# Performance work log

Hardware: AMD Instinct MI355X
Metric: run time of the kernel (lower is better)

The kernel has to match this reference:

```python
import jax, jax.numpy as jnp
import numpy as np

DIST_THD = 1.0   # config.dist_thd
EPS = 1e-8       # matches torch.nn.functional.cosine_similarity eps


def setup_inputs() -> dict:
    key = jax.random.key(0)
    k1, k2 = jax.random.split(key)
    async_fea = jax.random.normal(k1, (64, 512, 128), dtype=jnp.float32)  # [B, N, D]
    coord = jax.random.normal(k2, (64, 512, 2), dtype=jnp.float32)        # [B, N, 2]
    return {"async_fea": async_fea, "coord": coord}


def reference(async_fea, coord):
    B, N, _ = async_fea.shape
    # pairwise cosine similarity: normalize rows, then batched matmul
    norms = jnp.maximum(jnp.linalg.norm(async_fea, axis=-1, keepdims=True), EPS)
    fn = async_fea / norms
    cos = jnp.einsum('bid,bjd->bij', fn, fn)  # [B, N, N]

    # pairwise euclidean distance on coords
    diff = coord[:, :, None, :] - coord[:, None, :, :]  # [B, N, N, 2]
    d2 = jnp.sum(diff * diff, axis=-1)                   # [B, N, N]
    eye = jnp.eye(N, dtype=d2.dtype)
    # add eye before sqrt so the (zeroed-out) diagonal stays sqrt-safe
    dist = jnp.sqrt(d2 + eye)
    off_diag = 1.0 - eye

    async_adj = cos * jnp.exp(-dist / DIST_THD) * off_diag
    sync_adj = jnp.where(dist < DIST_THD, 1.0, 0.0) * off_diag
    return jnp.stack([async_adj, sync_adj])  # [2, B, N, N]
```

## Files before the change

### kernel.cpp

```cpp
#include <hip/hip_runtime.h>
#include <hip/hip_bf16.h>

typedef short bf16x8 __attribute__((ext_vector_type(8)));
typedef float f32x4  __attribute__((ext_vector_type(4)));

#define NB 64
#define NN 512
#define DD 128

__device__ __forceinline__ unsigned short f2bf(float f) {
    unsigned int u = __float_as_uint(f);
    unsigned int r = (u + 0x7FFFu + ((u >> 16) & 1u)) >> 16;
    return (unsigned short)r;
}

__global__ __launch_bounds__(256) void ASG_norm_kernel(
    const float* __restrict__ fea, unsigned int* __restrict__ fn)
{
    const int id   = blockIdx.x;
    const int xcd  = id & 7;
    const int q    = id >> 3;
    const int b    = xcd + 8 * (q >> 5);
    const int t    = q & 31;
    const int wid  = threadIdx.x >> 6;
    const int lane = threadIdx.x & 63;
    const int row0 = b * NN + t * 16 + wid * 4;
    const float2* src = reinterpret_cast<const float2*>(fea);

    float2 v[4];
    float  s[4];
#pragma unroll
    for (int rr = 0; rr < 4; ++rr) {
        v[rr] = src[(size_t)(row0 + rr) * (DD / 2) + lane];
        s[rr] = v[rr].x * v[rr].x + v[rr].y * v[rr].y;
    }
#pragma unroll
    for (int o = 32; o; o >>= 1) {
#pragma unroll
        for (int rr = 0; rr < 4; ++rr) s[rr] += __shfl_xor(s[rr], o);
    }
#pragma unroll
    for (int rr = 0; rr < 4; ++rr) {
        const float scale = 1.0f / fmaxf(sqrtf(s[rr]), 1e-8f);
        const unsigned short a = f2bf(v[rr].x * scale);
        const unsigned short bb = f2bf(v[rr].y * scale);
        fn[(size_t)(row0 + rr) * (DD / 2) + lane] =
            (unsigned int)a | ((unsigned int)bb << 16);
    }
}

__global__ __launch_bounds__(256, 4) void ASG_adj_kernel(
    const unsigned short* __restrict__ fn, const float* __restrict__ coord,
    float* __restrict__ out)
{
    const int id  = blockIdx.x;
    const int xcd = id & 7;
    const int q   = id >> 3;
    const int b   = xcd + 8 * (q >> 5);
    const int t   = q & 31;
    const int bi  = t >> 3;
    const int bj  = t & 7;

    const int tid = threadIdx.x;
    const int wid = tid >> 6, lane = tid & 63;
    const int wr  = wid >> 1, wc = wid & 1;
    const int row0 = bi * 128 + wr * 64;
    const int col0 = bj * 64  + wc * 32;
    const int lo = lane & 15, hi = lane >> 4;

    __shared__ float2 crow[128];
    __shared__ float2 ccol[64];
    __shared__ float  xpose[4][16 * 36];

    const float2* cb = reinterpret_cast<const float2*>(coord) + (size_t)b * NN;
    if (tid < 128)      crow[tid] = cb[bi * 128 + tid];
    else if (tid < 192) ccol[tid - 128] = cb[bj * 64 + (tid - 128)];
    __syncthreads();

    const unsigned short* fb = fn + (size_t)b * NN * DD;
    const int lk = hi * 8;

    bf16x8 bfrag[2][4];
#pragma unroll
    for (int n = 0; n < 2; ++n) {
        const unsigned short* p = fb + (size_t)(col0 + n * 16 + lo) * DD + lk;
#pragma unroll
        for (int kk = 0; kk < 4; ++kk)
            bfrag[n][kk] = *reinterpret_cast<const bf16x8*>(p + kk * 32);
    }

    float* outA = out + (size_t)b * NN * NN;
    float* outS = out + (size_t)NB * NN * NN + (size_t)b * NN * NN;
    float* xp = xpose[wid];

    const int c4 = (lane & 7) * 4;
    const int jbase = col0 + c4;
    float2 cj[4];
#pragma unroll
    for (int q2 = 0; q2 < 4; ++q2) cj[q2] = ccol[wc * 32 + c4 + q2];

#define LOADA(DST, MM)                                                        \
    {                                                                         \
        const unsigned short* p =                                             \
            fb + (size_t)(row0 + (MM) * 16 + lo) * DD + lk;                   \
        _Pragma("unroll")                                                     \
        for (int kk = 0; kk < 4; ++kk)                                        \
            DST[kk] = *reinterpret_cast<const bf16x8*>(p + kk * 32);          \
    }

#define STEP(MM, CURF, NEXTF, DO_PREF)                                        \
    {                                                                         \
        if (DO_PREF) LOADA(NEXTF, (MM) + 1);                                  \
        f32x4 acc[2];                                                         \
        _Pragma("unroll")                                                     \
        for (int n = 0; n < 2; ++n) acc[n] = (f32x4){0.f, 0.f, 0.f, 0.f};     \
        _Pragma("unroll")                                                     \
        for (int n = 0; n < 2; ++n)                                           \
            _Pragma("unroll")                                                 \
            for (int kk = 0; kk < 4; ++kk)                                    \
                acc[n] = __builtin_amdgcn_mfma_f32_16x16x32_bf16(             \
                    CURF[kk], bfrag[n][kk], acc[n], 0, 0, 0);                 \
                     \
        _Pragma("unroll")                                                     \
        for (int n = 0; n < 2; ++n)                                           \
            _Pragma("unroll")                                                 \
            for (int r = 0; r < 4; ++r)                                       \
                xp[(hi * 4 + r) * 36 + n * 16 + lo] = acc[n][r];              \
                \
        _Pragma("unroll")                                                     \
        for (int p2 = 0; p2 < 2; ++p2) {                                      \
            const int rr = p2 * 8 + (lane >> 3);         \
            const f32x4 cv =                                                  \
                *reinterpret_cast<const f32x4*>(&xp[rr * 36 + c4]);           \
            const int i = row0 + (MM) * 16 + rr;                              \
            const float2 ci = crow[wr * 64 + (MM) * 16 + rr];                 \
            f32x4 av, sv;                                                     \
            _Pragma("unroll")                                                 \
            for (int q2 = 0; q2 < 4; ++q2) {                                  \
                const int j = jbase + q2;                                     \
                     \
                const float dx = ci.x - cj[q2].x;                             \
                const float dy = ci.y - cj[q2].y;                             \
                const float d2 =                                              \
                    __fadd_rn(__fmul_rn(dx, dx), __fmul_rn(dy, dy));          \
                const float dist = __fsqrt_rn(d2);                            \
                const bool diag = (i == j);                                   \
                av[q2] = diag ? 0.0f : cv[q2] * __expf(-dist);                \
                sv[q2] = (!diag && dist < 1.0f) ? 1.0f : 0.0f;                \
            }                                                                 \
            const size_t off = (size_t)i * NN + jbase;                        \
            *reinterpret_cast<f32x4*>(outA + off) = av;                       \
            *reinterpret_cast<f32x4*>(outS + off) = sv;                       \
        }                                                                     \
    }

    bf16x8 af0[4], af1[4];
    LOADA(af0, 0);
    STEP(0, af0, af1, 1);
    STEP(1, af1, af0, 1);
    STEP(2, af0, af1, 1);
    STEP(3, af1, af0, 0);

#undef STEP
#undef LOADA
}

extern "C" void kernel_launch(void* const* d_in, const int* in_sizes, int n_in,
                              void* d_out, int out_size, void* d_ws, size_t ws_size,
                              hipStream_t stream) {
    const float* fea   = (const float*)d_in[0];
    const float* coord = (const float*)d_in[1];
    float* out = (float*)d_out;
    unsigned int* fn_ws = (unsigned int*)d_ws;

    ASG_norm_kernel<<<dim3(2048), 256, 0, stream>>>(fea, fn_ws);
    ASG_adj_kernel<<<dim3(2048), 256, 0, stream>>>(
        (const unsigned short*)fn_ws, coord, out);
}
```

Before: 40.81 us.

## Compute inverse row norms only and scale cosine after unnormalized bf16 matmul

The first kernel now only computes per-row reciprocal norms, no longer writing a normalized bf16 copy of the features. The adjacency kernel loads raw fp32 features, packs them to bf16 in registers with v_cvt_pk_bf16_f32, and applies the row and column inverse norms to the matmul result in the epilogue. This removes the bf16 workspace write and its re-read, but the adjacency kernel now reads twice as many bytes of fp32 features per fragment and does extra conversion work. Rounding of unnormalized features to bf16 also changes the numerics slightly.

```diff
diff --git a/kernel.cpp b/kernel.cpp
--- a/kernel.cpp
+++ b/kernel.cpp
@@ -8,50 +8,66 @@
 #define NN 512
 #define DD 128
 
-__device__ __forceinline__ unsigned short f2bf(float f) {
-    unsigned int u = __float_as_uint(f);
-    unsigned int r = (u + 0x7FFFu + ((u >> 16) & 1u)) >> 16;
-    return (unsigned short)r;
-}
-
-__global__ __launch_bounds__(256) void ASG_norm_kernel(
-    const float* __restrict__ fea, unsigned int* __restrict__ fn)
+__device__ __forceinline__ unsigned int cvt_pk_bf16(float lo, float hi) {
+    unsigned int r;
+    asm("v_cvt_pk_bf16_f32 %0, %1, %2" : "=v"(r) : "v"(lo), "v"(hi));
+    return r;
+}
+
+__device__ __forceinline__ bf16x8 load_frag8_f32(const float* __restrict__ p) {
+    const f32x4 a = *reinterpret_cast<const f32x4*>(p);
+    const f32x4 b = *reinterpret_cast<const f32x4*>(p + 4);
+    union { unsigned int u[4]; bf16x8 v; } r;
+    r.u[0] = cvt_pk_bf16(a[0], a[1]);
+    r.u[1] = cvt_pk_bf16(a[2], a[3]);
+    r.u[2] = cvt_pk_bf16(b[0], b[1]);
+    r.u[3] = cvt_pk_bf16(b[2], b[3]);
+    return r.v;
+}
+
+__global__ __launch_bounds__(256) void ASG_rs_kernel(
+    const float* __restrict__ fea, float* __restrict__ rs)
 {
-    const int id   = blockIdx.x;
-    const int xcd  = id & 7;
-    const int q    = id >> 3;
-    const int b    = xcd + 8 * (q >> 5);
-    const int t    = q & 31;
-    const int wid  = threadIdx.x >> 6;
-    const int lane = threadIdx.x & 63;
-    const int row0 = b * NN + t * 16 + wid * 4;
+    const int id  = blockIdx.x;
+    const int xcd = id & 7;
+    const int q   = id >> 3;
+    const int b   = xcd + 8 * (q >> 3);
+    const int t   = q & 7;
+    const int wid = threadIdx.x >> 6, lane = threadIdx.x & 63;
+    const int base = b * NN + t * 64;
+    const int row0 = base + wid * 16;
     const float2* src = reinterpret_cast<const float2*>(fea);
 
-    float2 v[4];
-    float  s[4];
-#pragma unroll
-    for (int rr = 0; rr < 4; ++rr) {
-        v[rr] = src[(size_t)(row0 + rr) * (DD / 2) + lane];
-        s[rr] = v[rr].x * v[rr].x + v[rr].y * v[rr].y;
-    }
-#pragma unroll
-    for (int o = 32; o; o >>= 1) {
-#pragma unroll
-        for (int rr = 0; rr < 4; ++rr) s[rr] += __shfl_xor(s[rr], o);
-    }
-#pragma unroll
-    for (int rr = 0; rr < 4; ++rr) {
-        const float scale = 1.0f / fmaxf(sqrtf(s[rr]), 1e-8f);
-        const unsigned short a = f2bf(v[rr].x * scale);
-        const unsigned short bb = f2bf(v[rr].y * scale);
-        fn[(size_t)(row0 + rr) * (DD / 2) + lane] =
-            (unsigned int)a | ((unsigned int)bb << 16);
-    }
+    __shared__ float lrs[64];
+
+#pragma unroll
+    for (int g = 0; g < 4; ++g) {
+        float2 v[4];
+        float  s[4];
+#pragma unroll
+        for (int rr = 0; rr < 4; ++rr) {
+            v[rr] = src[(size_t)(row0 + g * 4 + rr) * (DD / 2) + lane];
+            s[rr] = v[rr].x * v[rr].x + v[rr].y * v[rr].y;
+        }
+#pragma unroll
+        for (int o = 32; o; o >>= 1) {
+#pragma unroll
+            for (int rr = 0; rr < 4; ++rr) s[rr] += __shfl_xor(s[rr], o);
+        }
+        if (lane == 0) {
+#pragma unroll
+            for (int rr = 0; rr < 4; ++rr)
+                lrs[wid * 16 + g * 4 + rr] =
+                    1.0f / fmaxf(sqrtf(s[rr]), 1e-8f);
+        }
+    }
+    __syncthreads();
+    if (threadIdx.x < 64) rs[base + threadIdx.x] = lrs[threadIdx.x];
 }
 
 __global__ __launch_bounds__(256, 4) void ASG_adj_kernel(
-    const unsigned short* __restrict__ fn, const float* __restrict__ coord,
-    float* __restrict__ out)
+    const float* __restrict__ fea, const float* __restrict__ coord,
+    const float* __restrict__ rsbuf, float* __restrict__ out)
 {
     const int id  = blockIdx.x;
     const int xcd = id & 7;
@@ -70,23 +86,31 @@
 
     __shared__ float2 crow[128];
     __shared__ float2 ccol[64];
-    __shared__ float  xpose[4][16 * 36];
+    alignas(16) __shared__ float rsA[128];
+    alignas(16) __shared__ float rsB[64];
+    __shared__ float xpose[4][16 * 36];
 
     const float2* cb = reinterpret_cast<const float2*>(coord) + (size_t)b * NN;
-    if (tid < 128)      crow[tid] = cb[bi * 128 + tid];
-    else if (tid < 192) ccol[tid - 128] = cb[bj * 64 + (tid - 128)];
+    if (tid < 128) {
+        crow[tid] = cb[bi * 128 + tid];
+        rsA[tid]  = rsbuf[b * NN + bi * 128 + tid];
+    } else if (tid < 192) {
+        const int u = tid - 128;
+        ccol[u] = cb[bj * 64 + u];
+        rsB[u]  = rsbuf[b * NN + bj * 64 + u];
+    }
     __syncthreads();
 
-    const unsigned short* fb = fn + (size_t)b * NN * DD;
+    const float* feab = fea + (size_t)b * NN * DD;
     const int lk = hi * 8;
 
     bf16x8 bfrag[2][4];
 #pragma unroll
     for (int n = 0; n < 2; ++n) {
-        const unsigned short* p = fb + (size_t)(col0 + n * 16 + lo) * DD + lk;
+        const float* p = feab + (size_t)(col0 + n * 16 + lo) * DD + lk;
 #pragma unroll
         for (int kk = 0; kk < 4; ++kk)
-            bfrag[n][kk] = *reinterpret_cast<const bf16x8*>(p + kk * 32);
+            bfrag[n][kk] = load_frag8_f32(p + kk * 32);
     }
 
     float* outA = out + (size_t)b * NN * NN;
@@ -98,14 +122,14 @@
     float2 cj[4];
 #pragma unroll
     for (int q2 = 0; q2 < 4; ++q2) cj[q2] = ccol[wc * 32 + c4 + q2];
+    const f32x4 rsj = *reinterpret_cast<const f32x4*>(&rsB[wc * 32 + c4]);
 
 #define LOADA(DST, MM)                                                        \
     {                                                                         \
-        const unsigned short* p =                                             \
-            fb + (size_t)(row0 + (MM) * 16 + lo) * DD + lk;                   \
+        const float* p = feab + (size_t)(row0 + (MM) * 16 + lo) * DD + lk;    \
         _Pragma("unroll")                                                     \
         for (int kk = 0; kk < 4; ++kk)                                        \
-            DST[kk] = *reinterpret_cast<const bf16x8*>(p + kk * 32);          \
+            DST[kk] = load_frag8_f32(p + kk * 32);                            \
     }
 
 #define STEP(MM, CURF, NEXTF, DO_PREF)                                        \
@@ -133,6 +157,7 @@
             const f32x4 cv =                                                  \
                 *reinterpret_cast<const f32x4*>(&xp[rr * 36 + c4]);           \
             const int i = row0 + (MM) * 16 + rr;                              \
+            const float rsi = rsA[wr * 64 + (MM) * 16 + rr];                  \
             const float2 ci = crow[wr * 64 + (MM) * 16 + rr];                 \
             f32x4 av, sv;                                                     \
             _Pragma("unroll")                                                 \
@@ -145,7 +170,8 @@
                     __fadd_rn(__fmul_rn(dx, dx), __fmul_rn(dy, dy));          \
                 const float dist = __fsqrt_rn(d2);                            \
                 const bool diag = (i == j);                                   \
-                av[q2] = diag ? 0.0f : cv[q2] * __expf(-dist);                \
+                av[q2] = diag ? 0.0f                                          \
+                              : cv[q2] * rsi * rsj[q2] * __expf(-dist);       \
                 sv[q2] = (!diag && dist < 1.0f) ? 1.0f : 0.0f;                \
             }                                                                 \
             const size_t off = (size_t)i * NN + jbase;                        \
@@ -171,9 +197,8 @@
     const float* fea   = (const float*)d_in[0];
     const float* coord = (const float*)d_in[1];
     float* out = (float*)d_out;
-    unsigned int* fn_ws = (unsigned int*)d_ws;
-
-    ASG_norm_kernel<<<dim3(2048), 256, 0, stream>>>(fea, fn_ws);
-    ASG_adj_kernel<<<dim3(2048), 256, 0, stream>>>(
-        (const unsigned short*)fn_ws, coord, out);
-}
+    float* rs_ws = (float*)d_ws;
+
+    ASG_rs_kernel<<<dim3(512), 256, 0, stream>>>(fea, rs_ws);
+    ASG_adj_kernel<<<dim3(2048), 256, 0, stream>>>(fea, coord, rs_ws, out);
+}
```

New measurement: 66.42 us. 1.63x slower.

## Split sync adjacency output into a separate coordinate-only kernel

Applied to the files above, without the earlier changes.

Moves the thresholded sync adjacency computation and its store out of the MFMA kernel into a new third kernel that reads only coordinates and writes full 512-column rows. The async kernel now stores only the cosine-times-exp output, which lowers its store traffic and register pressure. The cost is an extra launch, recomputing the pairwise distances, and the sync kernel running serially after the async kernel on the same stream.

```diff
diff --git a/kernel.cpp b/kernel.cpp
--- a/kernel.cpp
+++ b/kernel.cpp
@@ -49,7 +49,7 @@
     }
 }
 
-__global__ __launch_bounds__(256, 4) void ASG_adj_kernel(
+__global__ __launch_bounds__(256, 4) void ASG_async_kernel(
     const unsigned short* __restrict__ fn, const float* __restrict__ coord,
     float* __restrict__ out)
 {
@@ -90,7 +90,6 @@
     }
 
     float* outA = out + (size_t)b * NN * NN;
-    float* outS = out + (size_t)NB * NN * NN + (size_t)b * NN * NN;
     float* xp = xpose[wid];
 
     const int c4 = (lane & 7) * 4;
@@ -120,13 +119,11 @@
             for (int kk = 0; kk < 4; ++kk)                                    \
                 acc[n] = __builtin_amdgcn_mfma_f32_16x16x32_bf16(             \
                     CURF[kk], bfrag[n][kk], acc[n], 0, 0, 0);                 \
-                     \
         _Pragma("unroll")                                                     \
         for (int n = 0; n < 2; ++n)                                           \
             _Pragma("unroll")                                                 \
             for (int r = 0; r < 4; ++r)                                       \
                 xp[(hi * 4 + r) * 36 + n * 16 + lo] = acc[n][r];              \
-                \
         _Pragma("unroll")                                                     \
         for (int p2 = 0; p2 < 2; ++p2) {                                      \
             const int rr = p2 * 8 + (lane >> 3);         \
@@ -134,7 +131,7 @@
                 *reinterpret_cast<const f32x4*>(&xp[rr * 36 + c4]);           \
             const int i = row0 + (MM) * 16 + rr;                              \
             const float2 ci = crow[wr * 64 + (MM) * 16 + rr];                 \
-            f32x4 av, sv;                                                     \
+            f32x4 av;                                                         \
             _Pragma("unroll")                                                 \
             for (int q2 = 0; q2 < 4; ++q2) {                                  \
                 const int j = jbase + q2;                                     \
@@ -146,11 +143,8 @@
                 const float dist = __fsqrt_rn(d2);                            \
                 const bool diag = (i == j);                                   \
                 av[q2] = diag ? 0.0f : cv[q2] * __expf(-dist);                \
-                sv[q2] = (!diag && dist < 1.0f) ? 1.0f : 0.0f;                \
             }                                                                 \
-            const size_t off = (size_t)i * NN + jbase;                        \
-            *reinterpret_cast<f32x4*>(outA + off) = av;                       \
-            *reinterpret_cast<f32x4*>(outS + off) = sv;                       \
+            *reinterpret_cast<f32x4*>(outA + (size_t)i * NN + jbase) = av;    \
         }                                                                     \
     }
 
@@ -163,6 +157,48 @@
 
 #undef STEP
 #undef LOADA
+}
+
+__global__ __launch_bounds__(256) void ASG_sync_kernel(
+    const float* __restrict__ coord, float* __restrict__ outS)
+{
+    const int bid = blockIdx.x;
+    const int b   = bid >> 5;
+    const int i0  = (bid & 31) * 16;
+    const int tid = threadIdx.x;
+
+    __shared__ float2 ccol[NN];
+    __shared__ float2 crow[16];
+    const float2* cb = reinterpret_cast<const float2*>(coord) + (size_t)b * NN;
+    ccol[tid]       = cb[tid];
+    ccol[tid + 256] = cb[tid + 256];
+    if (tid < 16) crow[tid] = cb[i0 + tid];
+    __syncthreads();
+
+    const int half = tid >> 7;
+    const int col  = (tid & 127) * 4;
+    float2 cj[4];
+#pragma unroll
+    for (int c = 0; c < 4; ++c) cj[c] = ccol[col + c];
+
+    float* o = outS + (size_t)b * NN * NN;
+#pragma unroll
+    for (int rr = 0; rr < 8; ++rr) {
+        const int lr = rr * 2 + half;
+        const int i  = i0 + lr;
+        const float2 ci = crow[lr];
+        f32x4 sv;
+#pragma unroll
+        for (int c = 0; c < 4; ++c) {
+            const float dx = ci.x - cj[c].x;
+            const float dy = ci.y - cj[c].y;
+            const float d2 = __fadd_rn(__fmul_rn(dx, dx), __fmul_rn(dy, dy));
+            const float dist = __fsqrt_rn(d2);
+            const bool diag = (i == col + c);
+            sv[c] = (!diag && dist < 1.0f) ? 1.0f : 0.0f;
+        }
+        *reinterpret_cast<f32x4*>(o + (size_t)i * NN + col) = sv;
+    }
 }
 
 extern "C" void kernel_launch(void* const* d_in, const int* in_sizes, int n_in,
@@ -174,6 +210,8 @@
     unsigned int* fn_ws = (unsigned int*)d_ws;
 
     ASG_norm_kernel<<<dim3(2048), 256, 0, stream>>>(fea, fn_ws);
-    ASG_adj_kernel<<<dim3(2048), 256, 0, stream>>>(
+    ASG_async_kernel<<<dim3(2048), 256, 0, stream>>>(
         (const unsigned short*)fn_ws, coord, out);
-}
+    ASG_sync_kernel<<<dim3(2048), 256, 0, stream>>>(
+        coord, out + (size_t)NB * NN * NN);
+}
```

After: 53.18 us. 30.3% more time.

## Stage async tile in shared LDS and write full 256-byte rows block-wide

Applied to the files above, without the earlier changes.

Replaces the per-wave 16x32 transpose buffer with a block-wide 128x68 LDS tile that holds the async adjacency values. After each half of the MFMA work, a block barrier lets every wave store 64-column row segments, giving wider contiguous global writes. The sync output is now computed in the store phase, which means distances are computed twice. This adds about 34KB of LDS, which may limit the launch_bounds occupancy target of 4 blocks, and adds two block-wide barriers that remove overlap between waves.

```diff
diff --git a/kernel.cpp b/kernel.cpp
--- a/kernel.cpp
+++ b/kernel.cpp
@@ -70,7 +70,7 @@
 
     __shared__ float2 crow[128];
     __shared__ float2 ccol[64];
-    __shared__ float  xpose[4][16 * 36];
+    __shared__ float  av_lds[128 * 68];
 
     const float2* cb = reinterpret_cast<const float2*>(coord) + (size_t)b * NN;
     if (tid < 128)      crow[tid] = cb[bi * 128 + tid];
@@ -91,13 +91,6 @@
 
     float* outA = out + (size_t)b * NN * NN;
     float* outS = out + (size_t)NB * NN * NN + (size_t)b * NN * NN;
-    float* xp = xpose[wid];
-
-    const int c4 = (lane & 7) * 4;
-    const int jbase = col0 + c4;
-    float2 cj[4];
-#pragma unroll
-    for (int q2 = 0; q2 < 4; ++q2) cj[q2] = ccol[wc * 32 + c4 + q2];
 
 #define LOADA(DST, MM)                                                        \
     {                                                                         \
@@ -108,7 +101,7 @@
             DST[kk] = *reinterpret_cast<const bf16x8*>(p + kk * 32);          \
     }
 
-#define STEP(MM, CURF, NEXTF, DO_PREF)                                        \
+#define CSTEP(MM, CURF, NEXTF, DO_PREF)                                       \
     {                                                                         \
         if (DO_PREF) LOADA(NEXTF, (MM) + 1);                                  \
         f32x4 acc[2];                                                         \
@@ -120,48 +113,75 @@
             for (int kk = 0; kk < 4; ++kk)                                    \
                 acc[n] = __builtin_amdgcn_mfma_f32_16x16x32_bf16(             \
                     CURF[kk], bfrag[n][kk], acc[n], 0, 0, 0);                 \
+        _Pragma("unroll")                                                     \
+        for (int n = 0; n < 2; ++n) {                                         \
+            const int lc = wc * 32 + n * 16 + lo;                             \
+            const int j  = bj * 64 + lc;                                      \
+            const float2 cj = ccol[lc];                                       \
+            _Pragma("unroll")                                                 \
+            for (int r = 0; r < 4; ++r) {                                     \
+                const int lr = wr * 64 + (MM) * 16 + hi * 4 + r;              \
+                const int i  = bi * 128 + lr;                                 \
+                const float2 ci = crow[lr];                                   \
                      \
-        _Pragma("unroll")                                                     \
-        for (int n = 0; n < 2; ++n)                                           \
-            _Pragma("unroll")                                                 \
-            for (int r = 0; r < 4; ++r)                                       \
-                xp[(hi * 4 + r) * 36 + n * 16 + lo] = acc[n][r];              \
-                \
-        _Pragma("unroll")                                                     \
-        for (int p2 = 0; p2 < 2; ++p2) {                                      \
-            const int rr = p2 * 8 + (lane >> 3);         \
-            const f32x4 cv =                                                  \
-                *reinterpret_cast<const f32x4*>(&xp[rr * 36 + c4]);           \
-            const int i = row0 + (MM) * 16 + rr;                              \
-            const float2 ci = crow[wr * 64 + (MM) * 16 + rr];                 \
-            f32x4 av, sv;                                                     \
-            _Pragma("unroll")                                                 \
-            for (int q2 = 0; q2 < 4; ++q2) {                                  \
-                const int j = jbase + q2;                                     \
-                     \
-                const float dx = ci.x - cj[q2].x;                             \
-                const float dy = ci.y - cj[q2].y;                             \
+                const float dx = ci.x - cj.x;                                 \
+                const float dy = ci.y - cj.y;                                 \
                 const float d2 =                                              \
                     __fadd_rn(__fmul_rn(dx, dx), __fmul_rn(dy, dy));          \
                 const float dist = __fsqrt_rn(d2);                            \
                 const bool diag = (i == j);                                   \
-                av[q2] = diag ? 0.0f : cv[q2] * __expf(-dist);                \
-                sv[q2] = (!diag && dist < 1.0f) ? 1.0f : 0.0f;                \
+                av_lds[lr * 68 + lc] =                                        \
+                    diag ? 0.0f : acc[n][r] * __expf(-dist);                  \
             }                                                                 \
-            const size_t off = (size_t)i * NN + jbase;                        \
-            *reinterpret_cast<f32x4*>(outA + off) = av;                       \
+        }                                                                     \
+    }
+
+    const int r4  = lane >> 4;
+    const int c4l = (lane & 15) * 4;
+    float2 cj2[4];
+#pragma unroll
+    for (int c = 0; c < 4; ++c) cj2[c] = ccol[c4l + c];
+    const int lrb0 = (wid & 1) * 64 + (wid >> 1) * 16;
+
+#define SSTEP(H)                                                              \
+    {                                                                         \
+        _Pragma("unroll")                                                     \
+        for (int p = 0; p < 4; ++p) {                                         \
+            const int lr = lrb0 + (H) * 32 + p * 4 + r4;                      \
+            const int gi = bi * 128 + lr;                                     \
+            const f32x4 av4 =                                                 \
+                *reinterpret_cast<const f32x4*>(&av_lds[lr * 68 + c4l]);      \
+            const size_t off = (size_t)gi * NN + bj * 64 + c4l;               \
+            *reinterpret_cast<f32x4*>(outA + off) = av4;                      \
+            const float2 ci = crow[lr];                                       \
+            f32x4 sv;                                                         \
+            _Pragma("unroll")                                                 \
+            for (int c = 0; c < 4; ++c) {                                     \
+                const float dx = ci.x - cj2[c].x;                             \
+                const float dy = ci.y - cj2[c].y;                             \
+                const float d2 =                                              \
+                    __fadd_rn(__fmul_rn(dx, dx), __fmul_rn(dy, dy));          \
+                const float dist = __fsqrt_rn(d2);                            \
+                const bool diag = (gi == bj * 64 + c4l + c);                  \
+                sv[c] = (!diag && dist < 1.0f) ? 1.0f : 0.0f;                 \
+            }                                                                 \
             *reinterpret_cast<f32x4*>(outS + off) = sv;                       \
         }                                                                     \
     }
 
     bf16x8 af0[4], af1[4];
     LOADA(af0, 0);
-    STEP(0, af0, af1, 1);
-    STEP(1, af1, af0, 1);
-    STEP(2, af0, af1, 1);
-    STEP(3, af1, af0, 0);
+    CSTEP(0, af0, af1, 1);
+    CSTEP(1, af1, af0, 1);
+    __syncthreads();
+    SSTEP(0);
+    CSTEP(2, af0, af1, 1);
+    CSTEP(3, af1, af0, 0);
+    __syncthreads();
+    SSTEP(1);
 
-#undef STEP
+#undef SSTEP
+#undef CSTEP
 #undef LOADA
 }
 
```

Measured after the change: 43.37 us. +6.3%, slower.
